# Kernel tuning notes

Hardware: AMD Instinct MI355X
Metric: run time of the kernel (lower is better)

Reference implementation:

```python
import jax, jax.numpy as jnp
import numpy as np

EV = 30  # choice_point


def _prelu(x, a):
    return jnp.where(x >= 0, x, a * x)


def setup_inputs() -> dict:
    key = jax.random.key(0)
    ks = jax.random.split(key, 7)
    n, c, h, w = 16, 64, 256, 256
    r = 2  # NonLocalAttention default reduction
    x = jax.random.normal(ks[0], (n, c, h, w), jnp.float32)
    # 1x1 conv weights (out_ch, in_ch) + bias + PReLU slope (scalar, torch default 0.25)
    W1 = jax.random.normal(ks[1], (c // r, c), jnp.float32) * 0.1
    b1 = jnp.zeros((c // r,), jnp.float32)
    a1 = jnp.array(0.25, jnp.float32)
    W2 = jax.random.normal(ks[2], (c // r, c), jnp.float32) * 0.1
    b2 = jnp.zeros((c // r,), jnp.float32)
    a2 = jnp.array(0.25, jnp.float32)
    Wa = jax.random.normal(ks[3], (c, c), jnp.float32) * 0.1
    ba = jnp.zeros((c,), jnp.float32)
    aa = jnp.array(0.25, jnp.float32)
    return {"input": x, "W1": W1, "b1": b1, "a1": a1,
            "W2": W2, "b2": b2, "a2": a2,
            "Wa": Wa, "ba": ba, "aa": aa}


def reference(input, W1, b1, a1, W2, b2, a2, Wa, ba, aa):
    n, c, h, w = input.shape
    hw = h * w
    L = EV * EV
    flat = input.reshape(n, c, hw)                       # [n,c,HW]
    # score per spatial position: count of channels with value >= 0
    z = jnp.sum(input >= 0, axis=1).reshape(n, hw)       # [n,HW] int
    idx = jnp.argsort(z, axis=-1)[:, :L]                 # [n,L] smallest counts first
    # gather selected positions across all channels
    q = jnp.take_along_axis(flat, idx[:, None, :], axis=-1)  # [n,c,L]
    # --- NonLocalAttention on the [n,c,EV,EV] patch (flattened spatial = L) ---
    e1 = _prelu(jnp.einsum('oc,ncl->nol', W1, q) + b1[None, :, None], a1)  # [n,c/2,L]
    e2 = _prelu(jnp.einsum('oc,ncl->nol', W2, q) + b2[None, :, None], a2)  # [n,c/2,L]
    ea = _prelu(jnp.einsum('oc,ncl->nol', Wa, q) + ba[None, :, None], aa)  # [n,c,L]
    score = jax.nn.softmax(jnp.einsum('ncl,ncm->nlm', e1, e2), axis=-1)    # [n,L,L]
    attn = jnp.einsum('nlm,ncm->ncl', score, ea)                           # [n,c,L]
    new_info = attn + q  # res_scale = 1
    # scatter the attended values back into the flat tensor
    bi = jnp.arange(n)[:, None, None]
    ci = jnp.arange(c)[None, :, None]
    out = flat.at[bi, ci, idx[:, None, :]].set(new_info)  # [n,c,HW]
    return out
```

## Files before the change

kernel.cpp:

```cpp
#include <hip/hip_runtime.h>
#include <hip/hip_fp16.h>

#define NB    16
#define CH    64
#define HWTOT 65536
#define LSEL  900
#define LPAD  912
#define KPAD  928

typedef _Float16 half8  __attribute__((ext_vector_type(8)));
typedef float    float4v __attribute__((ext_vector_type(4)));

#define OFF_HIST 0u
#define OFF_Z    5120u
#define OFF_IDX  1053696u
#define OFF_Q    1111296u
#define OFF_E1   4797696u
#define OFF_E2   5731584u
#define OFF_EA   6665472u

__global__ void k_copy_count(const float* __restrict__ x, float* __restrict__ out,
                             uchar4* __restrict__ z4, int* __restrict__ hist) {
    __shared__ int sh[65];
    int tid = threadIdx.x;
    if (tid < 65) sh[tid] = 0;
    __syncthreads();
    int b  = blockIdx.x >> 6;
    int wi = ((blockIdx.x & 63) << 8) | tid;
    const float4* xb = (const float4*)x + (size_t)b * CH * (HWTOT/4) + wi;
    float4*       ob = (float4*)out    + (size_t)b * CH * (HWTOT/4) + wi;
    int c0=0, c1=0, c2=0, c3=0;
    for (int c = 0; c < CH; ++c) {
        float4 v = xb[(size_t)c * (HWTOT/4)];
        ob[(size_t)c * (HWTOT/4)] = v;
        c0 += (v.x >= 0.f); c1 += (v.y >= 0.f);
        c2 += (v.z >= 0.f); c3 += (v.w >= 0.f);
    }
    z4[(size_t)b * (HWTOT/4) + wi] = make_uchar4((unsigned char)c0, (unsigned char)c1,
                                                 (unsigned char)c2, (unsigned char)c3);
    atomicAdd(&sh[c0], 1); atomicAdd(&sh[c1], 1);
    atomicAdd(&sh[c2], 1); atomicAdd(&sh[c3], 1);
    __syncthreads();
    if (tid < 65) atomicAdd(&hist[b*65 + tid], sh[tid]);
}

__global__ void k_select(const uchar4* __restrict__ z4, const int* __restrict__ hist,
                         int* __restrict__ idx) {
    int b = blockIdx.x;
    int cum = 0, t = 64, r = 0;
    for (int k = 0; k < 65; ++k) {
        int h = hist[b*65 + k];
        if (cum + h > LSEL) { t = k; r = LSEL - cum; break; }
        cum += h;
    }
    __shared__ int wsum[16];
    __shared__ int slot;
    int tid = threadIdx.x, lane = tid & 63, w = tid >> 6;
    if (tid == 0) slot = 0;
    __syncthreads();
    int run_eq = 0;
    const uchar4* zb = z4 + (size_t)b * (HWTOT/4);
    for (int chunk = 0; chunk < 16; ++chunk) {
        int i4 = (chunk << 10) | tid;
        uchar4 v = zb[i4];
        int e0 = (v.x == t), e1 = (v.y == t), e2 = (v.z == t), e3 = (v.w == t);
        int me = e0 + e1 + e2 + e3;
        int s = me;
        #pragma unroll
        for (int d = 1; d < 64; d <<= 1) {
            int u = __shfl_up(s, d, 64);
            if (lane >= d) s += u;
        }
        if (lane == 63) wsum[w] = s;
        __syncthreads();
        int woff = 0, tot = 0;
        for (int j = 0; j < 16; ++j) { int xx = wsum[j]; tot += xx; if (j < w) woff += xx; }
        int before = run_eq + woff + (s - me);
        int pos = i4 << 2;
        if ((v.x < t) || (e0 && (before            < r))) idx[b*LSEL + atomicAdd(&slot,1)] = pos;
        if ((v.y < t) || (e1 && (before+e0         < r))) idx[b*LSEL + atomicAdd(&slot,1)] = pos+1;
        if ((v.z < t) || (e2 && (before+e0+e1      < r))) idx[b*LSEL + atomicAdd(&slot,1)] = pos+2;
        if ((v.w < t) || (e3 && (before+e0+e1+e2   < r))) idx[b*LSEL + atomicAdd(&slot,1)] = pos+3;
        run_eq += tot;
        __syncthreads();
    }
}

__global__ void k_gather(const float* __restrict__ x, const int* __restrict__ idx,
                         float* __restrict__ q) {
    int g = blockIdx.x * 256 + threadIdx.x;
    int l = g % LSEL;
    int t = g / LSEL;
    int c = t & 63, b = t >> 6;
    int p = idx[b*LSEL + l];
    q[(size_t)(b*CH + c)*LSEL + l] = x[(size_t)(b*CH + c)*HWTOT + p];
}

#define E12_BLOCKS 3648
__global__ void k_e(const float* __restrict__ q,
                    const float* __restrict__ W1, const float* __restrict__ b1, const float* __restrict__ a1,
                    const float* __restrict__ W2, const float* __restrict__ b2, const float* __restrict__ a2,
                    const float* __restrict__ Wa, const float* __restrict__ ba, const float* __restrict__ aa,
                    _Float16* __restrict__ e1T, _Float16* __restrict__ e2T,
                    _Float16* __restrict__ eah) {
    if (blockIdx.x < E12_BLOCKS) {
        int g = blockIdx.x * 256 + threadIdx.x;
        int c = g & 31;
        int t = g >> 5;
        int l = t % LPAD; t /= LPAD;
        int which = t & 1, b = t >> 1;
        const float* W = which ? W2 : W1;
        float bias = which ? b2[c] : b1[c];
        float al   = which ? a2[0] : a1[0];
        float acc = 0.f;
        if (l < LSEL) {
            acc = bias;
            const float* qb = q + (size_t)b * CH * LSEL + l;
            for (int k = 0; k < CH; ++k) acc += W[c*CH + k] * qb[(size_t)k * LSEL];
            acc = (acc >= 0.f) ? acc : al * acc;
        }
        _Float16* e = which ? e2T : e1T;
        e[((size_t)b * LPAD + l) * 32 + c] = (_Float16)acc;
    } else {
        int bid = blockIdx.x - E12_BLOCKS;
        int c = bid & 63, b = bid >> 6;
        float bias = ba[c], al = aa[0];
        for (int m = threadIdx.x; m < KPAD; m += 256) {
            float acc = 0.f;
            if (m < LSEL) {
                acc = bias;
                const float* qb = q + (size_t)b * CH * LSEL + m;
                for (int k = 0; k < CH; ++k) acc += Wa[c*CH + k] * qb[(size_t)k * LSEL];
                acc = (acc >= 0.f) ? acc : al * acc;
            }
            eah[((size_t)b * CH + c) * KPAD + m] = (_Float16)acc;
        }
    }
}

__global__ __launch_bounds__(256, 2)
void k_attn(const _Float16* __restrict__ e1T, const _Float16* __restrict__ e2T,
            const _Float16* __restrict__ eah, const float* __restrict__ q,
            const int* __restrict__ idx, float* __restrict__ out) {
    int b = blockIdx.x / 57, tile = blockIdx.x % 57;
    int l0 = tile * 16;
    int tid = threadIdx.x, lane = tid & 63, w = tid >> 6;
    int n16 = lane & 15, quad = lane >> 4;

    __shared__ _Float16 pbuf[16][KPAD];
    __shared__ float rmx[4][16], rsm[4][16], rstat[16], rinv[16];

    pbuf[tid >> 4][LPAD + (tid & 15)] = (_Float16)0.f;

    half8 afrag = *(const half8*)(e1T + ((size_t)b*LPAD + l0 + n16)*32 + quad*8);

    float4v sv[15];
    const int nt = (w == 0) ? 15 : 14;
    #pragma unroll
    for (int i = 0; i < 15; ++i) {
        if (i < nt) {
            int t = w + 4*i;
            half8 bfrag = *(const half8*)(e2T + ((size_t)b*LPAD + t*16 + n16)*32 + quad*8);
            float4v z = {0.f, 0.f, 0.f, 0.f};
            sv[i] = __builtin_amdgcn_mfma_f32_16x16x32_f16(afrag, bfrag, z, 0, 0, 0);
        }
    }
    if (w == 0 && n16 >= 4) { sv[14][0] = sv[14][1] = sv[14][2] = sv[14][3] = -1e30f; }

    float mv0 = -1e30f, mv1 = -1e30f, mv2 = -1e30f, mv3 = -1e30f;
    #pragma unroll
    for (int i = 0; i < 15; ++i) if (i < nt) {
        mv0 = fmaxf(mv0, sv[i][0]); mv1 = fmaxf(mv1, sv[i][1]);
        mv2 = fmaxf(mv2, sv[i][2]); mv3 = fmaxf(mv3, sv[i][3]);
    }
    #pragma unroll
    for (int d = 1; d < 16; d <<= 1) {
        mv0 = fmaxf(mv0, __shfl_xor(mv0, d, 64));
        mv1 = fmaxf(mv1, __shfl_xor(mv1, d, 64));
        mv2 = fmaxf(mv2, __shfl_xor(mv2, d, 64));
        mv3 = fmaxf(mv3, __shfl_xor(mv3, d, 64));
    }
    if (n16 == 0) {
        rmx[w][quad*4+0] = mv0; rmx[w][quad*4+1] = mv1;
        rmx[w][quad*4+2] = mv2; rmx[w][quad*4+3] = mv3;
    }
    __syncthreads();
    if (tid < 16)
        rstat[tid] = fmaxf(fmaxf(rmx[0][tid], rmx[1][tid]), fmaxf(rmx[2][tid], rmx[3][tid]));
    __syncthreads();
    float rm0 = rstat[quad*4+0], rm1 = rstat[quad*4+1];
    float rm2 = rstat[quad*4+2], rm3 = rstat[quad*4+3];

    float s0 = 0.f, s1 = 0.f, s2 = 0.f, s3 = 0.f;
    #pragma unroll
    for (int i = 0; i < 15; ++i) if (i < nt) {
        int m = (w + 4*i)*16 + n16;
        float e0 = __expf(sv[i][0] - rm0); s0 += e0; pbuf[quad*4+0][m] = (_Float16)e0;
        float e1 = __expf(sv[i][1] - rm1); s1 += e1; pbuf[quad*4+1][m] = (_Float16)e1;
        float e2 = __expf(sv[i][2] - rm2); s2 += e2; pbuf[quad*4+2][m] = (_Float16)e2;
        float e3 = __expf(sv[i][3] - rm3); s3 += e3; pbuf[quad*4+3][m] = (_Float16)e3;
    }
    #pragma unroll
    for (int d = 1; d < 16; d <<= 1) {
        s0 += __shfl_xor(s0, d, 64); s1 += __shfl_xor(s1, d, 64);
        s2 += __shfl_xor(s2, d, 64); s3 += __shfl_xor(s3, d, 64);
    }
    if (n16 == 0) {
        rsm[w][quad*4+0] = s0; rsm[w][quad*4+1] = s1;
        rsm[w][quad*4+2] = s2; rsm[w][quad*4+3] = s3;
    }
    __syncthreads();
    if (tid < 16)
        rinv[tid] = 1.f / (rsm[0][tid] + rsm[1][tid] + rsm[2][tid] + rsm[3][tid]);
    __syncthreads();

    float4v acc0 = {0.f, 0.f, 0.f, 0.f}, acc1 = {0.f, 0.f, 0.f, 0.f};
    const _Float16* eb = eah + ((size_t)b*CH + w*16 + n16)*KPAD + quad*8;
    const _Float16* pb = &pbuf[n16][quad*8];
    #pragma unroll
    for (int k0 = 0; k0 < 896; k0 += 64) {
        half8 af0 = *(const half8*)(pb + k0);
        half8 bf0 = *(const half8*)(eb + k0);
        acc0 = __builtin_amdgcn_mfma_f32_16x16x32_f16(af0, bf0, acc0, 0, 0, 0);
        half8 af1 = *(const half8*)(pb + k0 + 32);
        half8 bf1 = *(const half8*)(eb + k0 + 32);
        acc1 = __builtin_amdgcn_mfma_f32_16x16x32_f16(af1, bf1, acc1, 0, 0, 0);
    }
    {
        half8 af = *(const half8*)(pb + 896);
        half8 bf = *(const half8*)(eb + 896);
        acc0 = __builtin_amdgcn_mfma_f32_16x16x32_f16(af, bf, acc0, 0, 0, 0);
    }

    int c = w*16 + n16;
    const float* qrow = q + (size_t)(b*CH + c)*LSEL;
    float* orow = out + (size_t)(b*CH + c)*HWTOT;
    const int* irow = idx + b*LSEL;
    #pragma unroll
    for (int v = 0; v < 4; ++v) {
        int lr = quad*4 + v;
        int l = l0 + lr;
        if (l < LSEL) {
            float val = (acc0[v] + acc1[v]) * rinv[lr] + qrow[l];
            orow[irow[l]] = val;
        }
    }
}

extern "C" void kernel_launch(void* const* d_in, const int* in_sizes, int n_in,
                              void* d_out, int out_size, void* d_ws, size_t ws_size,
                              hipStream_t stream) {
    const float* x  = (const float*)d_in[0];
    const float* W1 = (const float*)d_in[1];
    const float* b1 = (const float*)d_in[2];
    const float* a1 = (const float*)d_in[3];
    const float* W2 = (const float*)d_in[4];
    const float* b2 = (const float*)d_in[5];
    const float* a2 = (const float*)d_in[6];
    const float* Wa = (const float*)d_in[7];
    const float* ba = (const float*)d_in[8];
    const float* aa = (const float*)d_in[9];
    float* out = (float*)d_out;
    char* ws = (char*)d_ws;

    int*      hist = (int*)     (ws + OFF_HIST);
    uchar4*   z4   = (uchar4*)  (ws + OFF_Z);
    int*      idx  = (int*)     (ws + OFF_IDX);
    float*    q    = (float*)   (ws + OFF_Q);
    _Float16* e1T  = (_Float16*)(ws + OFF_E1);
    _Float16* e2T  = (_Float16*)(ws + OFF_E2);
    _Float16* eah  = (_Float16*)(ws + OFF_EA);

    hipMemsetAsync(hist, 0, NB*65*sizeof(int), stream);
    k_copy_count<<<NB*64, 256, 0, stream>>>(x, out, z4, hist);
    k_select<<<NB, 1024, 0, stream>>>(z4, hist, idx);
    k_gather<<<3600, 256, 0, stream>>>(x, idx, q);
    k_e<<<E12_BLOCKS + NB*CH, 256, 0, stream>>>(q, W1, b1, a1, W2, b2, a2,
                                                Wa, ba, aa, e1T, e2T, eah);
    k_attn<<<NB*57, 256, 0, stream>>>(e1T, e2T, eah, q, idx, out);
}
```

Measured before the change: 599.6 us.

## Fuse gather into projection kernel, drop memset and per-chunk syncs in select

Removes the separate gather kernel and q buffer: the projection kernel reads the selected positions straight from x through idx, and the attention epilogue reads the residual from x. Histograms are now written per block and summed in the select kernel, so the memset and global atomics go away. The select kernel loads all z values into registers first and computes wave offsets once, replacing sixteen rounds of block-wide synchronization. e1/e2 are computed together and each thread computes four ea channels, so loaded x values are reused; the cost is strided uncached gathers from x done several times.

```diff
diff --git a/kernel.cpp b/kernel.cpp
--- a/kernel.cpp
+++ b/kernel.cpp
@@ -11,16 +11,15 @@
 typedef _Float16 half8  __attribute__((ext_vector_type(8)));
 typedef float    float4v __attribute__((ext_vector_type(4)));
 
-#define OFF_HIST 0u
-#define OFF_Z    5120u
-#define OFF_IDX  1053696u
-#define OFF_Q    1111296u
-#define OFF_E1   4797696u
-#define OFF_E2   5731584u
-#define OFF_EA   6665472u
+#define OFF_HIST2 0u
+#define OFF_Z     270336u
+#define OFF_IDX   1318912u
+#define OFF_E1    1376512u
+#define OFF_E2    2310400u
+#define OFF_EA    3244288u
 
 __global__ void k_copy_count(const float* __restrict__ x, float* __restrict__ out,
-                             uchar4* __restrict__ z4, int* __restrict__ hist) {
+                             uchar4* __restrict__ z4, int* __restrict__ hist2) {
     __shared__ int sh[65];
     int tid = threadIdx.x;
     if (tid < 65) sh[tid] = 0;
@@ -41,29 +40,58 @@
     atomicAdd(&sh[c0], 1); atomicAdd(&sh[c1], 1);
     atomicAdd(&sh[c2], 1); atomicAdd(&sh[c3], 1);
     __syncthreads();
-    if (tid < 65) atomicAdd(&hist[b*65 + tid], sh[tid]);
-}
-
-__global__ void k_select(const uchar4* __restrict__ z4, const int* __restrict__ hist,
-                         int* __restrict__ idx) {
+    if (tid < 65) hist2[blockIdx.x * 65 + tid] = sh[tid];
+}
+
+__global__ void k_select(const unsigned int* __restrict__ zu_all,
+                         const int* __restrict__ hist2, int* __restrict__ idx) {
     int b = blockIdx.x;
+    int tid = threadIdx.x, lane = tid & 63, w = tid >> 6;
+    __shared__ int shh[65];
+    __shared__ int eqw[16];
+    __shared__ int slot;
+    if (tid == 0) slot = 0;
+    if (tid < 65) {
+        int h = 0;
+        #pragma unroll
+        for (int j = 0; j < 64; ++j) h += hist2[(b*64 + j)*65 + tid];
+        shh[tid] = h;
+    }
+    __syncthreads();
     int cum = 0, t = 64, r = 0;
     for (int k = 0; k < 65; ++k) {
-        int h = hist[b*65 + k];
+        int h = shh[k];
         if (cum + h > LSEL) { t = k; r = LSEL - cum; break; }
         cum += h;
     }
-    __shared__ int wsum[16];
-    __shared__ int slot;
-    int tid = threadIdx.x, lane = tid & 63, w = tid >> 6;
-    if (tid == 0) slot = 0;
-    __syncthreads();
-    int run_eq = 0;
-    const uchar4* zb = z4 + (size_t)b * (HWTOT/4);
-    for (int chunk = 0; chunk < 16; ++chunk) {
-        int i4 = (chunk << 10) | tid;
-        uchar4 v = zb[i4];
-        int e0 = (v.x == t), e1 = (v.y == t), e2 = (v.z == t), e3 = (v.w == t);
+    const unsigned int* zu = zu_all + (size_t)b * (HWTOT/4);
+    unsigned int zreg[16];
+    int mecnt = 0;
+    #pragma unroll
+    for (int g = 0; g < 16; ++g) {
+        unsigned int v = zu[(w << 10) | (g << 6) | lane];
+        zreg[g] = v;
+        mecnt += ((v      & 255u) == (unsigned)t);
+        mecnt += (((v>>8)  & 255u) == (unsigned)t);
+        mecnt += (((v>>16) & 255u) == (unsigned)t);
+        mecnt += (((v>>24) & 255u) == (unsigned)t);
+    }
+    int tot = mecnt;
+    #pragma unroll
+    for (int d = 1; d < 64; d <<= 1) tot += __shfl_xor(tot, d, 64);
+    if (lane == 0) eqw[w] = tot;
+    __syncthreads();
+    int eqbase = 0;
+    #pragma unroll
+    for (int j = 0; j < 16; ++j) { int xx = eqw[j]; if (j < w) eqbase += xx; }
+    int run = eqbase;
+    #pragma unroll
+    for (int g = 0; g < 16; ++g) {
+        unsigned int v = zreg[g];
+        int e0 = ((v      & 255u) == (unsigned)t);
+        int e1 = (((v>>8)  & 255u) == (unsigned)t);
+        int e2 = (((v>>16) & 255u) == (unsigned)t);
+        int e3 = (((v>>24) & 255u) == (unsigned)t);
         int me = e0 + e1 + e2 + e3;
         int s = me;
         #pragma unroll
@@ -71,33 +99,24 @@
             int u = __shfl_up(s, d, 64);
             if (lane >= d) s += u;
         }
-        if (lane == 63) wsum[w] = s;
-        __syncthreads();
-        int woff = 0, tot = 0;
-        for (int j = 0; j < 16; ++j) { int xx = wsum[j]; tot += xx; if (j < w) woff += xx; }
-        int before = run_eq + woff + (s - me);
+        int before = run + (s - me);
+        int i4 = (w << 10) | (g << 6) | lane;
         int pos = i4 << 2;
-        if ((v.x < t) || (e0 && (before            < r))) idx[b*LSEL + atomicAdd(&slot,1)] = pos;
-        if ((v.y < t) || (e1 && (before+e0         < r))) idx[b*LSEL + atomicAdd(&slot,1)] = pos+1;
-        if ((v.z < t) || (e2 && (before+e0+e1      < r))) idx[b*LSEL + atomicAdd(&slot,1)] = pos+2;
-        if ((v.w < t) || (e3 && (before+e0+e1+e2   < r))) idx[b*LSEL + atomicAdd(&slot,1)] = pos+3;
-        run_eq += tot;
-        __syncthreads();
-    }
-}
-
-__global__ void k_gather(const float* __restrict__ x, const int* __restrict__ idx,
-                         float* __restrict__ q) {
-    int g = blockIdx.x * 256 + threadIdx.x;
-    int l = g % LSEL;
-    int t = g / LSEL;
-    int c = t & 63, b = t >> 6;
-    int p = idx[b*LSEL + l];
-    q[(size_t)(b*CH + c)*LSEL + l] = x[(size_t)(b*CH + c)*HWTOT + p];
-}
-
-#define E12_BLOCKS 3648
-__global__ void k_e(const float* __restrict__ q,
+        int b0 = ((v      & 255u) < (unsigned)t);
+        int b1 = (((v>>8)  & 255u) < (unsigned)t);
+        int b2 = (((v>>16) & 255u) < (unsigned)t);
+        int b3 = (((v>>24) & 255u) < (unsigned)t);
+        if (b0 || (e0 && (before            < r))) idx[b*LSEL + atomicAdd(&slot,1)] = pos;
+        if (b1 || (e1 && (before+e0         < r))) idx[b*LSEL + atomicAdd(&slot,1)] = pos+1;
+        if (b2 || (e2 && (before+e0+e1      < r))) idx[b*LSEL + atomicAdd(&slot,1)] = pos+2;
+        if (b3 || (e3 && (before+e0+e1+e2   < r))) idx[b*LSEL + atomicAdd(&slot,1)] = pos+3;
+        run += __shfl(s, 63, 64);
+    }
+}
+
+#define E12_BLOCKS 1824
+#define EA_BLOCKS  928
+__global__ void k_e(const float* __restrict__ x, const int* __restrict__ idx,
                     const float* __restrict__ W1, const float* __restrict__ b1, const float* __restrict__ a1,
                     const float* __restrict__ W2, const float* __restrict__ b2, const float* __restrict__ a2,
                     const float* __restrict__ Wa, const float* __restrict__ ba, const float* __restrict__ aa,
@@ -107,40 +126,60 @@
         int g = blockIdx.x * 256 + threadIdx.x;
         int c = g & 31;
         int t = g >> 5;
-        int l = t % LPAD; t /= LPAD;
-        int which = t & 1, b = t >> 1;
-        const float* W = which ? W2 : W1;
-        float bias = which ? b2[c] : b1[c];
-        float al   = which ? a2[0] : a1[0];
-        float acc = 0.f;
+        int l = t % LPAD;
+        int b = t / LPAD;
+        float acc1 = 0.f, acc2 = 0.f;
         if (l < LSEL) {
-            acc = bias;
-            const float* qb = q + (size_t)b * CH * LSEL + l;
-            for (int k = 0; k < CH; ++k) acc += W[c*CH + k] * qb[(size_t)k * LSEL];
-            acc = (acc >= 0.f) ? acc : al * acc;
-        }
-        _Float16* e = which ? e2T : e1T;
-        e[((size_t)b * LPAD + l) * 32 + c] = (_Float16)acc;
+            int p = idx[b*LSEL + l];
+            acc1 = b1[c]; acc2 = b2[c];
+            const float* xb = x + (size_t)b * CH * HWTOT + p;
+            #pragma unroll 8
+            for (int k = 0; k < CH; ++k) {
+                float xv = xb[(size_t)k * HWTOT];
+                acc1 += W1[c*CH + k] * xv;
+                acc2 += W2[c*CH + k] * xv;
+            }
+            float al1 = a1[0], al2 = a2[0];
+            acc1 = (acc1 >= 0.f) ? acc1 : al1 * acc1;
+            acc2 = (acc2 >= 0.f) ? acc2 : al2 * acc2;
+        }
+        e1T[((size_t)b * LPAD + l) * 32 + c] = (_Float16)acc1;
+        e2T[((size_t)b * LPAD + l) * 32 + c] = (_Float16)acc2;
     } else {
         int bid = blockIdx.x - E12_BLOCKS;
-        int c = bid & 63, b = bid >> 6;
-        float bias = ba[c], al = aa[0];
-        for (int m = threadIdx.x; m < KPAD; m += 256) {
-            float acc = 0.f;
-            if (m < LSEL) {
-                acc = bias;
-                const float* qb = q + (size_t)b * CH * LSEL + m;
-                for (int k = 0; k < CH; ++k) acc += Wa[c*CH + k] * qb[(size_t)k * LSEL];
-                acc = (acc >= 0.f) ? acc : al * acc;
+        int b  = bid / 58;
+        int mt = bid % 58;
+        int m  = mt*16 + (threadIdx.x & 15);
+        int c0 = (threadIdx.x >> 4) * 4;
+        float a0 = 0.f, a1v = 0.f, a2v = 0.f, a3v = 0.f;
+        if (m < LSEL) {
+            int p = idx[b*LSEL + m];
+            a0 = ba[c0]; a1v = ba[c0+1]; a2v = ba[c0+2]; a3v = ba[c0+3];
+            const float* xb = x + (size_t)b * CH * HWTOT + p;
+            #pragma unroll 8
+            for (int k = 0; k < CH; ++k) {
+                float xv = xb[(size_t)k * HWTOT];
+                a0  += Wa[(c0  )*CH + k] * xv;
+                a1v += Wa[(c0+1)*CH + k] * xv;
+                a2v += Wa[(c0+2)*CH + k] * xv;
+                a3v += Wa[(c0+3)*CH + k] * xv;
             }
-            eah[((size_t)b * CH + c) * KPAD + m] = (_Float16)acc;
-        }
+            float al = aa[0];
+            a0  = (a0  >= 0.f) ? a0  : al * a0;
+            a1v = (a1v >= 0.f) ? a1v : al * a1v;
+            a2v = (a2v >= 0.f) ? a2v : al * a2v;
+            a3v = (a3v >= 0.f) ? a3v : al * a3v;
+        }
+        eah[((size_t)b * CH + c0  ) * KPAD + m] = (_Float16)a0;
+        eah[((size_t)b * CH + c0+1) * KPAD + m] = (_Float16)a1v;
+        eah[((size_t)b * CH + c0+2) * KPAD + m] = (_Float16)a2v;
+        eah[((size_t)b * CH + c0+3) * KPAD + m] = (_Float16)a3v;
     }
 }
 
 __global__ __launch_bounds__(256, 2)
 void k_attn(const _Float16* __restrict__ e1T, const _Float16* __restrict__ e2T,
-            const _Float16* __restrict__ eah, const float* __restrict__ q,
+            const _Float16* __restrict__ eah, const float* __restrict__ x,
             const int* __restrict__ idx, float* __restrict__ out) {
     int b = blockIdx.x / 57, tile = blockIdx.x % 57;
     int l0 = tile * 16;
@@ -233,7 +272,7 @@
     }
 
     int c = w*16 + n16;
-    const float* qrow = q + (size_t)(b*CH + c)*LSEL;
+    const float* xrow = x + (size_t)(b*CH + c)*HWTOT;
     float* orow = out + (size_t)(b*CH + c)*HWTOT;
     const int* irow = idx + b*LSEL;
     #pragma unroll
@@ -241,8 +280,9 @@
         int lr = quad*4 + v;
         int l = l0 + lr;
         if (l < LSEL) {
-            float val = (acc0[v] + acc1[v]) * rinv[lr] + qrow[l];
-            orow[irow[l]] = val;
+            int p = irow[l];
+            float val = (acc0[v] + acc1[v]) * rinv[lr] + xrow[p];
+            orow[p] = val;
         }
     }
 }
@@ -263,19 +303,17 @@
     float* out = (float*)d_out;
     char* ws = (char*)d_ws;
 
-    int*      hist = (int*)     (ws + OFF_HIST);
-    uchar4*   z4   = (uchar4*)  (ws + OFF_Z);
-    int*      idx  = (int*)     (ws + OFF_IDX);
-    float*    q    = (float*)   (ws + OFF_Q);
-    _Float16* e1T  = (_Float16*)(ws + OFF_E1);
-    _Float16* e2T  = (_Float16*)(ws + OFF_E2);
-    _Float16* eah  = (_Float16*)(ws + OFF_EA);
-
-    hipMemsetAsync(hist, 0, NB*65*sizeof(int), stream);
-    k_copy_count<<<NB*64, 256, 0, stream>>>(x, out, z4, hist);
-    k_select<<<NB, 1024, 0, stream>>>(z4, hist, idx);
-    k_gather<<<3600, 256, 0, stream>>>(x, idx, q);
-    k_e<<<E12_BLOCKS + NB*CH, 256, 0, stream>>>(q, W1, b1, a1, W2, b2, a2,
-                                                Wa, ba, aa, e1T, e2T, eah);
-    k_attn<<<NB*57, 256, 0, stream>>>(e1T, e2T, eah, q, idx, out);
-}
+    int*          hist2 = (int*)         (ws + OFF_HIST2);
+    uchar4*       z4    = (uchar4*)      (ws + OFF_Z);
+    unsigned int* zu    = (unsigned int*)(ws + OFF_Z);
+    int*          idx   = (int*)         (ws + OFF_IDX);
+    _Float16*     e1T   = (_Float16*)    (ws + OFF_E1);
+    _Float16*     e2T   = (_Float16*)    (ws + OFF_E2);
+    _Float16*     eah   = (_Float16*)    (ws + OFF_EA);
+
+    k_copy_count<<<NB*64, 256, 0, stream>>>(x, out, z4, hist2);
+    k_select<<<NB, 1024, 0, stream>>>(zu, hist2, idx);
+    k_e<<<E12_BLOCKS + EA_BLOCKS, 256, 0, stream>>>(x, idx, W1, b1, a1, W2, b2, a2,
+                                                    Wa, ba, aa, e1T, e2T, eah);
+    k_attn<<<NB*57, 256, 0, stream>>>(e1T, e2T, eah, x, idx, out);
+}
```

Result: faster. 587.5 us (-2.0%).
